# Kernel optimization log

Hardware: AMD Instinct MI355X
Metric: run time of the kernel (lower is better)

## Reference

```python
import jax, jax.numpy as jnp
import numpy as np

QMAX = 127.0

def setup_inputs() -> dict:
    key = jax.random.key(0)
    kx, kw, ks = jax.random.split(key, 3)
    B, S, D_IN, D_OUT = 4, 2048, 4096, 4096
    x = jax.random.normal(kx, (B, S, D_IN), dtype=jnp.float16)
    # int8 weight buffer, same distribution as torch.randint(-127, 127)
    weight = jax.random.randint(kw, (D_OUT, D_IN), -127, 127, dtype=jnp.int32).astype(jnp.int8)
    # per-output-channel weight scales (fp16 buffer); small positive values
    weight_scales = (jax.random.uniform(ks, (D_OUT,), dtype=jnp.float32) * 0.01 + 1e-4).astype(jnp.float16)
    return {"x": x, "weight": weight, "weight_scales": weight_scales}

def reference(x, weight, weight_scales):
    # x: [B, S, D_in] fp16; weight: [D_out, D_in] int8; weight_scales: [D_out] fp16
    x32 = x.astype(jnp.float32)
    # dynamic per-token absmax quantization: scale = absmax / 127
    absmax = jnp.max(jnp.abs(x32), axis=-1, keepdims=True)      # [B, S, 1]
    x_scales = jnp.maximum(absmax / QMAX, 1e-8)
    q = jnp.round(x32 / x_scales)                                # in [-127, 127]
    q = jnp.clip(q, -QMAX, QMAX).astype(jnp.int8)
    # int8 GEMM accumulated in int32 (cupy.matmul on int32 in the original)
    y = jnp.einsum('bsk,nk->bsn', q.astype(jnp.int32), weight.astype(jnp.int32),
                   preferred_element_type=jnp.int32)             # [B, S, D_out]
    # dequant: per-token activation scale * per-channel weight scale
    y = y.astype(jnp.float32) * x_scales * weight_scales.astype(jnp.float32)[None, None, :]
    return y.astype(jnp.float16)
```

## Files before the change

kernel.cpp:

```cpp
#include <hip/hip_runtime.h>
#include <stdint.h>

typedef int int32x4 __attribute__((ext_vector_type(4)));

constexpr int K_DIM = 4096;
constexpr int N_DIM = 4096;
constexpr float QMAXF = 127.0f;

__global__ __launch_bounds__(256) void quant_rows(const float* __restrict__ x,
                                                  int8_t* __restrict__ q,
                                                  float* __restrict__ scales) {
    const int row = blockIdx.x;
    const int tid = threadIdx.x;
    const size_t base = (size_t)row * K_DIM;

    const float4* xv = reinterpret_cast<const float4*>(x + base);
    float4 v[4];
#pragma unroll
    for (int i = 0; i < 4; ++i) v[i] = xv[tid + 256 * i];

    float m = 0.0f;
#pragma unroll
    for (int i = 0; i < 4; ++i)
        m = fmaxf(m, fmaxf(fmaxf(fabsf(v[i].x), fabsf(v[i].y)),
                           fmaxf(fabsf(v[i].z), fabsf(v[i].w))));
#pragma unroll
    for (int off = 32; off > 0; off >>= 1) m = fmaxf(m, __shfl_xor(m, off));

    __shared__ float wmax[4];
    if ((tid & 63) == 0) wmax[tid >> 6] = m;
    __syncthreads();
    const float am = fmaxf(fmaxf(wmax[0], wmax[1]), fmaxf(wmax[2], wmax[3]));
    const float scale = fmaxf(am * (1.0f / 127.0f), 1e-8f);
    if (tid == 0) scales[row] = scale;
    const float inv = 1.0f / scale;

    int* qw = reinterpret_cast<int*>(q + base);
#pragma unroll
    for (int i = 0; i < 4; ++i) {
        float f0 = fminf(QMAXF, fmaxf(-QMAXF, rintf(v[i].x * inv)));
        float f1 = fminf(QMAXF, fmaxf(-QMAXF, rintf(v[i].y * inv)));
        float f2 = fminf(QMAXF, fmaxf(-QMAXF, rintf(v[i].z * inv)));
        float f3 = fminf(QMAXF, fmaxf(-QMAXF, rintf(v[i].w * inv)));
        int b0 = ((int)f0) & 255, b1 = ((int)f1) & 255;
        int b2 = ((int)f2) & 255, b3 = ((int)f3) & 255;
        qw[tid + 256 * i] = b0 | (b1 << 8) | (b2 << 16) | (b3 << 24);
    }
}

__global__ __launch_bounds__(256) void pack_w(const int* __restrict__ w,
                                              int8_t* __restrict__ w8) {
    const int idx = blockIdx.x * 256 + threadIdx.x;
    const int4 v = reinterpret_cast<const int4*>(w)[idx];
    int packed = (v.x & 255) | ((v.y & 255) << 8) | ((v.z & 255) << 16) | ((v.w & 255) << 24);
    reinterpret_cast<int*>(w8)[idx] = packed;
}

constexpr int BM = 256, BN = 256, BKB = 128;
constexpr int NT = K_DIM / BKB;

#define GLL(src, dst)                                                          \
    __builtin_amdgcn_global_load_lds(                                          \
        (const __attribute__((address_space(1))) unsigned int*)(src),          \
        (__attribute__((address_space(3))) unsigned int*)(dst), 16, 0, 0)

#define MFMA_I8(a, b, c) __builtin_amdgcn_mfma_i32_16x16x64_i8((a), (b), (c), 0, 0, 0)

__global__ __launch_bounds__(512, 2) void w8a8_gemm256(
        const int8_t* __restrict__ A, const int8_t* __restrict__ B,
        const float* __restrict__ asc, const float* __restrict__ wsc,
        float* __restrict__ C, int M) {
    extern __shared__ int8_t lds[];

    const int tid  = threadIdx.x;
    const int lane = tid & 63;
    const int wave = tid >> 6;

    const int nwg = gridDim.x;
    const int bid = blockIdx.x;
    const int swz = (bid & 7) * (nwg >> 3) + (bid >> 3);
    const int NB  = N_DIM / BN;
    const int brow = (swz / NB) * BM;
    const int bcol = (swz % NB) * BN;

    const int wm = wave >> 2;
    const int wn = wave & 3;
    const int l15 = lane & 15;
    const int ls  = lane >> 4;

    const int rowin = tid >> 3;
    const int gsl   = ((tid & 7) ^ (rowin & 7)) * 16;
    const int8_t* gA = A + (size_t)(brow + rowin) * K_DIM + gsl;
    const int8_t* gB = B + (size_t)(bcol + rowin) * K_DIM + gsl;
    const size_t chunk_g = (size_t)64 * K_DIM;
    const int segb = wave * 1024;

    const int sbase = ((ls ^ (l15 & 7)) * 16);
    const int offA0 = (wm * 128 + l15) * BKB + sbase;
    const int offB0 = (wn * 64  + l15) * BKB + sbase;

    int32x4 acc[8][4];
#pragma unroll
    for (int i = 0; i < 8; ++i)
#pragma unroll
        for (int j = 0; j < 4; ++j) acc[i][j] = (int32x4){0, 0, 0, 0};

#pragma unroll
    for (int c = 0; c < 4; ++c) GLL(gA + c * chunk_g, lds + c * 8192 + segb);
#pragma unroll
    for (int c = 0; c < 4; ++c) GLL(gB + c * chunk_g, lds + 65536 + c * 8192 + segb);

    int32x4 bf[4][2];
    int32x4 afr[3][2];

    for (int t = 0; t < NT; ++t) {
        const int8_t* Ab = lds + (t & 1) * 32768;
        const int8_t* Bb = lds + 65536 + (t & 1) * 32768;
        int8_t* dA = lds + ((t + 1) & 1) * 32768;
        int8_t* dB = lds + 65536 + ((t + 1) & 1) * 32768;
        const bool pf = (t + 1 < NT);
        const size_t kk = (size_t)(t + 1) * BKB;

        __builtin_amdgcn_s_barrier();
        if (pf) {
#pragma unroll
            for (int c = 0; c < 4; ++c) GLL(gA + kk + c * chunk_g, dA + c * 8192 + segb);
            asm volatile("s_waitcnt vmcnt(4)" ::: "memory");
        } else {
            asm volatile("s_waitcnt vmcnt(0)" ::: "memory");
        }
        __builtin_amdgcn_s_barrier();

#pragma unroll
        for (int ni = 0; ni < 4; ++ni) {
            bf[ni][0] = *(const int32x4*)(Bb + ((offB0 + ni * 2048)));
            bf[ni][1] = *(const int32x4*)(Bb + ((offB0 + ni * 2048) ^ 64));
        }
#pragma unroll
        for (int mi = 0; mi < 2; ++mi) {
            afr[mi][0] = *(const int32x4*)(Ab + ((offA0 + mi * 2048)));
            afr[mi][1] = *(const int32x4*)(Ab + ((offA0 + mi * 2048) ^ 64));
        }

#pragma unroll
        for (int mi = 0; mi < 8; ++mi) {
            if (mi < 6) {
                const int s = (mi + 2) % 3;
                afr[s][0] = *(const int32x4*)(Ab + ((offA0 + (mi + 2) * 2048)));
                afr[s][1] = *(const int32x4*)(Ab + ((offA0 + (mi + 2) * 2048) ^ 64));
            }
            if (mi == 4 && pf) {
#pragma unroll
                for (int c = 0; c < 4; ++c)
                    GLL(gB + kk + c * chunk_g, dB + c * 8192 + segb);
            }
            if (mi < 6)      asm volatile("s_waitcnt lgkmcnt(4)" ::: "memory");
            else if (mi == 6) asm volatile("s_waitcnt lgkmcnt(2)" ::: "memory");
            else              asm volatile("s_waitcnt lgkmcnt(0)" ::: "memory");
            __builtin_amdgcn_sched_barrier(0);

            const int cs = mi % 3;
            __builtin_amdgcn_s_setprio(1);
#pragma unroll
            for (int ni = 0; ni < 4; ++ni) {
                acc[mi][ni] = MFMA_I8(afr[cs][0], bf[ni][0], acc[mi][ni]);
                acc[mi][ni] = MFMA_I8(afr[cs][1], bf[ni][1], acc[mi][ni]);
            }
            __builtin_amdgcn_s_setprio(0);
        }
    }

    const int c0  = lane & 15;
    const int rr0 = (lane >> 4) * 4;
#pragma unroll
    for (int ni = 0; ni < 4; ++ni) {
        const int col = bcol + wn * 64 + ni * 16 + c0;
        const float ws = wsc[col];
#pragma unroll
        for (int mi = 0; mi < 8; ++mi) {
            const int rowb = brow + wm * 128 + mi * 16 + rr0;
#pragma unroll
            for (int r = 0; r < 4; ++r) {
                const int row = rowb + r;
                float o = (float)acc[mi][ni][r] * asc[row] * ws;
                o = (float)(_Float16)o;
                C[(size_t)row * N_DIM + col] = o;
            }
        }
    }
}

extern "C" void kernel_launch(void* const* d_in, const int* in_sizes, int n_in,
                              void* d_out, int out_size, void* d_ws, size_t ws_size,
                              hipStream_t stream) {
    const float* x   = (const float*)d_in[0];
    const int*   w   = (const int*)d_in[1];
    const float* wsc = (const float*)d_in[2];
    float* out = (float*)d_out;

    const int K = K_DIM;
    const int M = in_sizes[0] / K;
    const int N = N_DIM;

    int8_t* q   = (int8_t*)d_ws;
    int8_t* w8  = (int8_t*)d_ws + (size_t)M * K;
    float*  asc = (float*)((char*)d_ws + (size_t)M * K + (size_t)N * K);

    quant_rows<<<M, 256, 0, stream>>>(x, q, asc);
    pack_w<<<(N * (K / 4)) / 256, 256, 0, stream>>>(w, w8);
    const int grid = (M / BM) * (N / BN);
    w8a8_gemm256<<<grid, 512, 131072, stream>>>(q, w8, asc, wsc, out, M);
}
```

Measured before the change: 182.5 us.

## Switch int8 GEMM to 32x32x32 MFMA tiles with reworked LDS fragment schedule

Replaces the 16x16x64 int8 MFMA tiling with 32x32x32 int8 MFMAs. Each wave now holds a 4x2 grid of 32x32 accumulators, and the matching LDS fragment loads, swizzle and epilogue index mapping are rewritten to suit. The larger instruction is meant to cut LDS fragment reads and instruction-issue overhead per FLOP. The manual lgkmcnt waits are dropped and a full vmcnt(0) wait plus barrier is added before the loop, so overlapping LDS reads with MFMAs is left to the compiler. This risks losing overlap or raising register pressure.

```diff
diff --git a/kernel.cpp b/kernel.cpp
--- a/kernel.cpp
+++ b/kernel.cpp
@@ -1,7 +1,8 @@
 #include <hip/hip_runtime.h>
 #include <stdint.h>
 
-typedef int int32x4 __attribute__((ext_vector_type(4)));
+typedef int int32x4  __attribute__((ext_vector_type(4)));
+typedef int int32x16 __attribute__((ext_vector_type(16)));
 
 constexpr int K_DIM = 4096;
 constexpr int N_DIM = 4096;
@@ -64,7 +65,17 @@
         (const __attribute__((address_space(1))) unsigned int*)(src),          \
         (__attribute__((address_space(3))) unsigned int*)(dst), 16, 0, 0)
 
-#define MFMA_I8(a, b, c) __builtin_amdgcn_mfma_i32_16x16x64_i8((a), (b), (c), 0, 0, 0)
+#define MFMA32(a, b, c) __builtin_amdgcn_mfma_i32_32x32x32_i8((a), (b), (c), 0, 0, 0)
+
+#define MFMA4(ACC, AF, BF)                                                     \
+    {                                                                          \
+        __builtin_amdgcn_s_setprio(1);                                         \
+        ACC = MFMA32(AF[0], BF[0], ACC);                                       \
+        ACC = MFMA32(AF[1], BF[1], ACC);                                       \
+        ACC = MFMA32(AF[2], BF[2], ACC);                                       \
+        ACC = MFMA32(AF[3], BF[3], ACC);                                       \
+        __builtin_amdgcn_s_setprio(0);                                         \
+    }
 
 __global__ __launch_bounds__(512, 2) void w8a8_gemm256(
         const int8_t* __restrict__ A, const int8_t* __restrict__ B,
@@ -85,8 +96,8 @@
 
     const int wm = wave >> 2;
     const int wn = wave & 3;
-    const int l15 = lane & 15;
-    const int ls  = lane >> 4;
+    const int l31 = lane & 31;
+    const int lh  = lane >> 5;
 
     const int rowin = tid >> 3;
     const int gsl   = ((tid & 7) ^ (rowin & 7)) * 16;
@@ -95,23 +106,27 @@
     const size_t chunk_g = (size_t)64 * K_DIM;
     const int segb = wave * 1024;
 
-    const int sbase = ((ls ^ (l15 & 7)) * 16);
-    const int offA0 = (wm * 128 + l15) * BKB + sbase;
-    const int offB0 = (wn * 64  + l15) * BKB + sbase;
-
-    int32x4 acc[8][4];
-#pragma unroll
-    for (int i = 0; i < 8; ++i)
-#pragma unroll
-        for (int j = 0; j < 4; ++j) acc[i][j] = (int32x4){0, 0, 0, 0};
-
-#pragma unroll
-    for (int c = 0; c < 4; ++c) GLL(gA + c * chunk_g, lds + c * 8192 + segb);
-#pragma unroll
-    for (int c = 0; c < 4; ++c) GLL(gB + c * chunk_g, lds + 65536 + c * 8192 + segb);
-
-    int32x4 bf[4][2];
-    int32x4 afr[3][2];
+    const int sb = lh ^ (l31 & 7);
+    const int baseA = (wm * 128 + l31) * BKB;
+    const int baseB = (wn * 64  + l31) * BKB;
+
+    int32x16 acc[4][2];
+#pragma unroll
+    for (int i = 0; i < 4; ++i)
+#pragma unroll
+        for (int j = 0; j < 2; ++j)
+#pragma unroll
+            for (int e = 0; e < 16; ++e) acc[i][j][e] = 0;
+
+#pragma unroll
+    for (int c = 0; c < 4; ++c) {
+        GLL(gA + c * chunk_g, lds + c * 8192 + segb);
+        GLL(gB + c * chunk_g, lds + 65536 + c * 8192 + segb);
+    }
+    asm volatile("s_waitcnt vmcnt(0)" ::: "memory");
+    __builtin_amdgcn_s_barrier();
+
+    int32x4 af[2][4], bf[2][4];
 
     for (int t = 0; t < NT; ++t) {
         const int8_t* Ab = lds + (t & 1) * 32768;
@@ -124,7 +139,8 @@
         __builtin_amdgcn_s_barrier();
         if (pf) {
 #pragma unroll
-            for (int c = 0; c < 4; ++c) GLL(gA + kk + c * chunk_g, dA + c * 8192 + segb);
+            for (int c = 0; c < 4; ++c)
+                GLL(gA + kk + c * chunk_g, dA + c * 8192 + segb);
             asm volatile("s_waitcnt vmcnt(4)" ::: "memory");
         } else {
             asm volatile("s_waitcnt vmcnt(0)" ::: "memory");
@@ -132,56 +148,54 @@
         __builtin_amdgcn_s_barrier();
 
 #pragma unroll
-        for (int ni = 0; ni < 4; ++ni) {
-            bf[ni][0] = *(const int32x4*)(Bb + ((offB0 + ni * 2048)));
-            bf[ni][1] = *(const int32x4*)(Bb + ((offB0 + ni * 2048) ^ 64));
-        }
-#pragma unroll
-        for (int mi = 0; mi < 2; ++mi) {
-            afr[mi][0] = *(const int32x4*)(Ab + ((offA0 + mi * 2048)));
-            afr[mi][1] = *(const int32x4*)(Ab + ((offA0 + mi * 2048) ^ 64));
-        }
-
-#pragma unroll
-        for (int mi = 0; mi < 8; ++mi) {
-            if (mi < 6) {
-                const int s = (mi + 2) % 3;
-                afr[s][0] = *(const int32x4*)(Ab + ((offA0 + (mi + 2) * 2048)));
-                afr[s][1] = *(const int32x4*)(Ab + ((offA0 + (mi + 2) * 2048) ^ 64));
-            }
-            if (mi == 4 && pf) {
-#pragma unroll
-                for (int c = 0; c < 4; ++c)
-                    GLL(gB + kk + c * chunk_g, dB + c * 8192 + segb);
-            }
-            if (mi < 6)      asm volatile("s_waitcnt lgkmcnt(4)" ::: "memory");
-            else if (mi == 6) asm volatile("s_waitcnt lgkmcnt(2)" ::: "memory");
-            else              asm volatile("s_waitcnt lgkmcnt(0)" ::: "memory");
-            __builtin_amdgcn_sched_barrier(0);
-
-            const int cs = mi % 3;
-            __builtin_amdgcn_s_setprio(1);
-#pragma unroll
-            for (int ni = 0; ni < 4; ++ni) {
-                acc[mi][ni] = MFMA_I8(afr[cs][0], bf[ni][0], acc[mi][ni]);
-                acc[mi][ni] = MFMA_I8(afr[cs][1], bf[ni][1], acc[mi][ni]);
-            }
-            __builtin_amdgcn_s_setprio(0);
-        }
-    }
-
-    const int c0  = lane & 15;
-    const int rr0 = (lane >> 4) * 4;
-#pragma unroll
-    for (int ni = 0; ni < 4; ++ni) {
-        const int col = bcol + wn * 64 + ni * 16 + c0;
+        for (int ks = 0; ks < 4; ++ks) {
+            af[0][ks] = *(const int32x4*)(Ab + baseA + ((sb ^ (2 * ks)) * 16));
+            bf[0][ks] = *(const int32x4*)(Bb + baseB + ((sb ^ (2 * ks)) * 16));
+        }
+
+#pragma unroll
+        for (int ks = 0; ks < 4; ++ks)
+            bf[1][ks] = *(const int32x4*)(Bb + baseB + 4096 + ((sb ^ (2 * ks)) * 16));
+        MFMA4(acc[0][0], af[0], bf[0]);
+
+#pragma unroll
+        for (int ks = 0; ks < 4; ++ks)
+            af[1][ks] = *(const int32x4*)(Ab + baseA + 4096 + ((sb ^ (2 * ks)) * 16));
+        MFMA4(acc[0][1], af[0], bf[1]);
+
+#pragma unroll
+        for (int ks = 0; ks < 4; ++ks)
+            af[0][ks] = *(const int32x4*)(Ab + baseA + 8192 + ((sb ^ (2 * ks)) * 16));
+        MFMA4(acc[1][0], af[1], bf[0]);
+
+        MFMA4(acc[1][1], af[1], bf[1]);
+
+#pragma unroll
+        for (int ks = 0; ks < 4; ++ks)
+            af[1][ks] = *(const int32x4*)(Ab + baseA + 12288 + ((sb ^ (2 * ks)) * 16));
+        MFMA4(acc[2][0], af[0], bf[0]);
+
+        if (pf) {
+#pragma unroll
+            for (int c = 0; c < 4; ++c)
+                GLL(gB + kk + c * chunk_g, dB + c * 8192 + segb);
+        }
+        MFMA4(acc[2][1], af[0], bf[1]);
+
+        MFMA4(acc[3][0], af[1], bf[0]);
+        MFMA4(acc[3][1], af[1], bf[1]);
+    }
+
+#pragma unroll
+    for (int ni = 0; ni < 2; ++ni) {
+        const int col = bcol + wn * 64 + ni * 32 + l31;
         const float ws = wsc[col];
 #pragma unroll
-        for (int mi = 0; mi < 8; ++mi) {
-            const int rowb = brow + wm * 128 + mi * 16 + rr0;
-#pragma unroll
-            for (int r = 0; r < 4; ++r) {
-                const int row = rowb + r;
+        for (int mi = 0; mi < 4; ++mi) {
+            const int rowb = brow + wm * 128 + mi * 32 + 4 * lh;
+#pragma unroll
+            for (int r = 0; r < 16; ++r) {
+                const int row = rowb + (r & 3) + 8 * (r >> 2);
                 float o = (float)acc[mi][ni][r] * asc[row] * ws;
                 o = (float)(_Float16)o;
                 C[(size_t)row * N_DIM + col] = o;
```

Result: slower. 197.3 us (+8.1%).

## Load A fragments directly from global to registers, triple-buffer B in LDS

Applied to the files above, without the earlier changes.

Each wave now loads its A fragments straight from global memory into registers, double-buffered across tiles, so A no longer passes through LDS. Only B is staged in LDS, now in a three-slot ring with two-tile lookahead. The wave layout changes to 4x2 with 64x128 wave tiles, and LDS use drops from 128KB to 96KB. This cuts LDS traffic and barrier pressure, but each A row is now fetched from global or L2 by every wave that needs it, with uncoalesced 16-byte row reads and more register pressure.

```diff
diff --git a/kernel.cpp b/kernel.cpp
--- a/kernel.cpp
+++ b/kernel.cpp
@@ -58,6 +58,7 @@
 
 constexpr int BM = 256, BN = 256, BKB = 128;
 constexpr int NT = K_DIM / BKB;
+constexpr int BSLOT = 32768;
 
 #define GLL(src, dst)                                                          \
     __builtin_amdgcn_global_load_lds(                                          \
@@ -66,7 +67,7 @@
 
 #define MFMA_I8(a, b, c) __builtin_amdgcn_mfma_i32_16x16x64_i8((a), (b), (c), 0, 0, 0)
 
-__global__ __launch_bounds__(512, 2) void w8a8_gemm256(
+__global__ __launch_bounds__(512, 2) void w8a8_flat(
         const int8_t* __restrict__ A, const int8_t* __restrict__ B,
         const float* __restrict__ asc, const float* __restrict__ wsc,
         float* __restrict__ C, int M) {
@@ -83,102 +84,102 @@
     const int brow = (swz / NB) * BM;
     const int bcol = (swz % NB) * BN;
 
-    const int wm = wave >> 2;
-    const int wn = wave & 3;
+    const int wm = wave & 3;
+    const int wn = wave >> 2;
     const int l15 = lane & 15;
     const int ls  = lane >> 4;
 
-    const int rowin = tid >> 3;
-    const int gsl   = ((tid & 7) ^ (rowin & 7)) * 16;
-    const int8_t* gA = A + (size_t)(brow + rowin) * K_DIM + gsl;
-    const int8_t* gB = B + (size_t)(bcol + rowin) * K_DIM + gsl;
-    const size_t chunk_g = (size_t)64 * K_DIM;
+    const int8_t* aglob = A + (size_t)(brow + wm * 64 + l15) * K_DIM + ls * 16;
+
+    const int rowst = tid >> 3;
+    const int gsl   = ((tid & 7) ^ (rowst & 7)) * 16;
+    const int8_t* gB = B + (size_t)(bcol + rowst) * K_DIM + gsl;
+    const size_t chB = (size_t)64 * K_DIM;
     const int segb = wave * 1024;
 
-    const int sbase = ((ls ^ (l15 & 7)) * 16);
-    const int offA0 = (wm * 128 + l15) * BKB + sbase;
-    const int offB0 = (wn * 64  + l15) * BKB + sbase;
-
-    int32x4 acc[8][4];
-#pragma unroll
-    for (int i = 0; i < 8; ++i)
-#pragma unroll
-        for (int j = 0; j < 4; ++j) acc[i][j] = (int32x4){0, 0, 0, 0};
-
-#pragma unroll
-    for (int c = 0; c < 4; ++c) GLL(gA + c * chunk_g, lds + c * 8192 + segb);
-#pragma unroll
-    for (int c = 0; c < 4; ++c) GLL(gB + c * chunk_g, lds + 65536 + c * 8192 + segb);
-
-    int32x4 bf[4][2];
-    int32x4 afr[3][2];
-
-    for (int t = 0; t < NT; ++t) {
-        const int8_t* Ab = lds + (t & 1) * 32768;
-        const int8_t* Bb = lds + 65536 + (t & 1) * 32768;
-        int8_t* dA = lds + ((t + 1) & 1) * 32768;
-        int8_t* dB = lds + 65536 + ((t + 1) & 1) * 32768;
-        const bool pf = (t + 1 < NT);
-        const size_t kk = (size_t)(t + 1) * BKB;
-
-        __builtin_amdgcn_s_barrier();
-        if (pf) {
-#pragma unroll
-            for (int c = 0; c < 4; ++c) GLL(gA + kk + c * chunk_g, dA + c * 8192 + segb);
-            asm volatile("s_waitcnt vmcnt(4)" ::: "memory");
-        } else {
-            asm volatile("s_waitcnt vmcnt(0)" ::: "memory");
-        }
-        __builtin_amdgcn_s_barrier();
-
-#pragma unroll
-        for (int ni = 0; ni < 4; ++ni) {
-            bf[ni][0] = *(const int32x4*)(Bb + ((offB0 + ni * 2048)));
-            bf[ni][1] = *(const int32x4*)(Bb + ((offB0 + ni * 2048) ^ 64));
-        }
-#pragma unroll
-        for (int mi = 0; mi < 2; ++mi) {
-            afr[mi][0] = *(const int32x4*)(Ab + ((offA0 + mi * 2048)));
-            afr[mi][1] = *(const int32x4*)(Ab + ((offA0 + mi * 2048) ^ 64));
-        }
-
-#pragma unroll
-        for (int mi = 0; mi < 8; ++mi) {
-            if (mi < 6) {
-                const int s = (mi + 2) % 3;
-                afr[s][0] = *(const int32x4*)(Ab + ((offA0 + (mi + 2) * 2048)));
-                afr[s][1] = *(const int32x4*)(Ab + ((offA0 + (mi + 2) * 2048) ^ 64));
-            }
-            if (mi == 4 && pf) {
-#pragma unroll
-                for (int c = 0; c < 4; ++c)
-                    GLL(gB + kk + c * chunk_g, dB + c * 8192 + segb);
-            }
-            if (mi < 6)      asm volatile("s_waitcnt lgkmcnt(4)" ::: "memory");
-            else if (mi == 6) asm volatile("s_waitcnt lgkmcnt(2)" ::: "memory");
-            else              asm volatile("s_waitcnt lgkmcnt(0)" ::: "memory");
-            __builtin_amdgcn_sched_barrier(0);
-
-            const int cs = mi % 3;
-            __builtin_amdgcn_s_setprio(1);
-#pragma unroll
-            for (int ni = 0; ni < 4; ++ni) {
-                acc[mi][ni] = MFMA_I8(afr[cs][0], bf[ni][0], acc[mi][ni]);
-                acc[mi][ni] = MFMA_I8(afr[cs][1], bf[ni][1], acc[mi][ni]);
-            }
-            __builtin_amdgcn_s_setprio(0);
-        }
+    const int boff = (wn * 128 + l15) * BKB + ((ls ^ (l15 & 7)) * 16);
+
+    int32x4 acc[4][8];
+#pragma unroll
+    for (int i = 0; i < 4; ++i)
+#pragma unroll
+        for (int j = 0; j < 8; ++j) acc[i][j] = (int32x4){0, 0, 0, 0};
+
+    int32x4 avA[8], avB[8];
+
+#pragma unroll
+    for (int mi = 0; mi < 4; ++mi) {
+        avA[2 * mi]     = *(const int32x4*)(aglob + (size_t)mi * 16 * K_DIM);
+        avA[2 * mi + 1] = *(const int32x4*)(aglob + (size_t)mi * 16 * K_DIM + 64);
+    }
+#pragma unroll
+    for (int c = 0; c < 4; ++c) GLL(gB + c * chB, lds + c * 8192 + segb);
+#pragma unroll
+    for (int c = 0; c < 4; ++c) GLL(gB + 128 + c * chB, lds + BSLOT + c * 8192 + segb);
+    asm volatile("s_waitcnt vmcnt(4)" ::: "memory");
+    __builtin_amdgcn_s_barrier();
+
+#define TILE_BODY(T, AVC, AVN)                                                 \
+    {                                                                          \
+        const int8_t* Bb = lds + ((T) % 3) * BSLOT;                            \
+        const bool pf1 = ((T) + 1 < NT);                                       \
+        const bool pf2 = ((T) + 2 < NT);                                       \
+        int32x4 bf[2][2];                                                      \
+        bf[0][0] = *(const int32x4*)(Bb + boff);                               \
+        bf[0][1] = *(const int32x4*)(Bb + (boff ^ 64));                        \
+        _Pragma("unroll")                                                      \
+        for (int ni = 0; ni < 8; ++ni) {                                       \
+            const int cur = ni & 1, nxt = cur ^ 1;                             \
+            if (ni < 4 && pf1) {                                               \
+                const int8_t* ap = aglob + ((T) + 1) * 128 +                   \
+                                   (size_t)ni * 16 * K_DIM;                    \
+                AVN[2 * ni]     = *(const int32x4*)(ap);                       \
+                AVN[2 * ni + 1] = *(const int32x4*)(ap + 64);                  \
+            }                                                                  \
+            if (ni == 4 && pf2) {                                              \
+                int8_t* dst = lds + (((T) + 2) % 3) * BSLOT;                   \
+                _Pragma("unroll")                                              \
+                for (int c = 0; c < 4; ++c)                                    \
+                    GLL(gB + ((T) + 2) * 128 + c * chB,                        \
+                        dst + c * 8192 + segb);                                \
+            }                                                                  \
+            if (ni < 7) {                                                      \
+                const int o = boff + (ni + 1) * 2048;                          \
+                bf[nxt][0] = *(const int32x4*)(Bb + o);                        \
+                bf[nxt][1] = *(const int32x4*)(Bb + (o ^ 64));                 \
+                asm volatile("s_waitcnt lgkmcnt(2)" ::: "memory");             \
+            } else {                                                           \
+                asm volatile("s_waitcnt lgkmcnt(0)" ::: "memory");             \
+            }                                                                  \
+            __builtin_amdgcn_sched_barrier(0);                                 \
+            __builtin_amdgcn_s_setprio(1);                                     \
+            _Pragma("unroll")                                                  \
+            for (int mi = 0; mi < 4; ++mi) {                                   \
+                acc[mi][ni] = MFMA_I8(AVC[2 * mi], bf[cur][0], acc[mi][ni]);   \
+                acc[mi][ni] = MFMA_I8(AVC[2 * mi + 1], bf[cur][1], acc[mi][ni]); \
+            }                                                                  \
+            __builtin_amdgcn_s_setprio(0);                                     \
+        }                                                                      \
+        if ((T) <= NT - 3) asm volatile("s_waitcnt vmcnt(4)" ::: "memory");    \
+        else               asm volatile("s_waitcnt vmcnt(0)" ::: "memory");    \
+        __builtin_amdgcn_sched_barrier(0);                                     \
+        __builtin_amdgcn_s_barrier();                                          \
+    }
+
+    for (int t = 0; t < NT; t += 2) {
+        TILE_BODY(t,     avA, avB);
+        TILE_BODY(t + 1, avB, avA);
     }
 
     const int c0  = lane & 15;
     const int rr0 = (lane >> 4) * 4;
 #pragma unroll
-    for (int ni = 0; ni < 4; ++ni) {
-        const int col = bcol + wn * 64 + ni * 16 + c0;
+    for (int ni = 0; ni < 8; ++ni) {
+        const int col = bcol + wn * 128 + ni * 16 + c0;
         const float ws = wsc[col];
 #pragma unroll
-        for (int mi = 0; mi < 8; ++mi) {
-            const int rowb = brow + wm * 128 + mi * 16 + rr0;
+        for (int mi = 0; mi < 4; ++mi) {
+            const int rowb = brow + wm * 64 + mi * 16 + rr0;
 #pragma unroll
             for (int r = 0; r < 4; ++r) {
                 const int row = rowb + r;
@@ -209,5 +210,5 @@
     quant_rows<<<M, 256, 0, stream>>>(x, q, asc);
     pack_w<<<(N * (K / 4)) / 256, 256, 0, stream>>>(w, w8);
     const int grid = (M / BM) * (N / BN);
-    w8a8_gemm256<<<grid, 512, 131072, stream>>>(q, w8, asc, wsc, out, M);
-}
+    w8a8_flat<<<grid, 512, 98304, stream>>>(q, w8, asc, wsc, out, M);
+}
```

Result: slower. 222.5 us (+21.9%).
